# Kernel tuning notes

Hardware: AMD Instinct MI355X
Metric: run time of the kernel (lower is better)

The kernel has to match this reference:

```python
import jax, jax.numpy as jnp
import numpy as np

WINDOW = 8
HEADS = 8

def _rel_index(w):
    coords = np.stack(np.meshgrid(np.arange(w), np.arange(w), indexing='ij')).reshape(2, -1)
    rel = coords[:, :, None] - coords[:, None, :]          # [2, N, N]
    rel = rel.transpose(1, 2, 0) + (w - 1)                 # [N, N, 2]
    return jnp.asarray(rel[:, :, 0] * (2 * w - 1) + rel[:, :, 1])  # [N, N] int

def setup_inputs() -> dict:
    key = jax.random.key(0)
    ks = jax.random.split(key, 5)
    B, N, C = 4096, WINDOW * WINDOW, 256
    x = jax.random.normal(ks[0], (B, N, C), dtype=jnp.float32)
    w_qkv = jax.random.normal(ks[1], (3 * C, C), dtype=jnp.float32) * 0.02
    b_qkv = jnp.zeros((3 * C,), dtype=jnp.float32)
    bias_table = jax.random.normal(ks[2], ((2 * WINDOW - 1) ** 2, HEADS), dtype=jnp.float32) * 0.02
    w_proj = jax.random.normal(ks[3], (C, C), dtype=jnp.float32) * 0.02
    b_proj = jnp.zeros((C,), dtype=jnp.float32)
    return {"x": x, "w_qkv": w_qkv, "b_qkv": b_qkv, "bias_table": bias_table,
            "w_proj": w_proj, "b_proj": b_proj}

def reference(x, w_qkv, b_qkv, bias_table, w_proj, b_proj):
    B, N, C = x.shape
    H = HEADS
    d = C // H
    scale = d ** (-0.5)
    idx = _rel_index(WINDOW)                                # [N, N]
    qkv = x @ w_qkv.T + b_qkv                               # [B, N, 3C]
    qkv = qkv.reshape(B, N, 3, H, d).transpose(2, 0, 3, 1, 4)
    q, k, v = qkv[0], qkv[1], qkv[2]                        # [B, H, N, d]
    attn = jnp.einsum('bhnd,bhmd->bhnm', q * scale, k)      # [B, H, N, N]
    bias = bias_table[idx]                                  # [N, N, H]
    attn = attn + bias.transpose(2, 0, 1)[None]             # add per-head bias
    attn = jax.nn.softmax(attn, axis=-1)
    out = jnp.einsum('bhnm,bhmd->bhnd', attn, v)            # [B, H, N, d]
    out = out.transpose(0, 2, 1, 3).reshape(B, N, C)
    return out @ w_proj.T + b_proj
```

## Files before the change

### kernel.cpp

```cpp
#include <hip/hip_runtime.h>

typedef unsigned int u32;
typedef unsigned short u16;
typedef __bf16 bf16x8 __attribute__((ext_vector_type(8)));
typedef float f32x4 __attribute__((ext_vector_type(4)));
typedef u32 u32x4 __attribute__((ext_vector_type(4)));
typedef u32 u32x2 __attribute__((ext_vector_type(2)));

#define NTOK 64
#define CDIM 256
#define NH 8

#define WS_HDR 8
#define BIAS_O (WS_HDR)
#define WQKV_O (BIAS_O + 32768)
#define BQKV_O (WQKV_O + 196608)
#define WPRJ_O (BQKV_O + 768)
#define BPRJ_O (WPRJ_O + 65536)

#define XROW 520
#define XS_OFF 0
#define QS_OFF 33280
#define KS_OFF 66560
#define VT_OFF 99840
#define LDS_BYTES 134656

__device__ __forceinline__ float bf2f(u16 u) {
  union { u32 i; float f; } z; z.i = ((u32)u) << 16; return z.f;
}
__device__ __forceinline__ u16 f2bf(float f) {
  __bf16 h = (__bf16)f; return __builtin_bit_cast(u16, h);
}
__device__ __forceinline__ float fetchf(const void* p, int idx, int isbf) {
  return isbf ? bf2f(((const u16*)p)[idx]) : ((const float*)p)[idx];
}

__global__ void detect_dtype(const u16* __restrict__ x, int* __restrict__ flag) {
  __shared__ int cnt;
  if (threadIdx.x == 0) cnt = 0;
  __syncthreads();
  int sane = 0;
  for (int i = threadIdx.x; i < 2048; i += 256) {
    u16 u = x[2 * i];
    int e = (u >> 7) & 0xFF;
    sane += (e == 0 || (e >= 90 && e <= 160)) ? 1 : 0;
  }
  atomicAdd(&cnt, sane);
  __syncthreads();
  if (threadIdx.x == 0) *flag = (cnt >= 1638) ? 1 : 0;
}

__global__ void cvt_params(const void* __restrict__ wqkv, const void* __restrict__ bqkv,
                           const void* __restrict__ btab, const void* __restrict__ wprj,
                           const void* __restrict__ bprj, void* __restrict__ wsraw) {
  u16* ws = (u16*)wsraw;
  const int isbf = *(const int*)wsraw;
  int i = blockIdx.x * 256 + threadIdx.x;
  if (i < 32768) {
    int h = i >> 12, n = (i >> 6) & 63, m = i & 63;
    int r0 = (n >> 3) - (m >> 3) + 7, r1 = (n & 7) - (m & 7) + 7;
    ws[BIAS_O + (h << 12) + (m << 6) + n] = f2bf(fetchf(btab, (r0 * 15 + r1) * NH + h, isbf));
  } else if (i < 32768 + 196608) {
    int j = i - 32768;
    ws[WQKV_O + j] = f2bf(fetchf(wqkv, j, isbf));
  } else if (i < 32768 + 196608 + 768) {
    int j = i - (32768 + 196608);
    ws[BQKV_O + j] = f2bf(fetchf(bqkv, j, isbf));
  } else if (i < 32768 + 196608 + 768 + 65536) {
    int j = i - (32768 + 196608 + 768);
    ws[WPRJ_O + j] = f2bf(fetchf(wprj, j, isbf));
  } else if (i < 32768 + 196608 + 768 + 65536 + 256) {
    int j = i - (32768 + 196608 + 768 + 65536);
    ws[BPRJ_O + j] = f2bf(fetchf(bprj, j, isbf));
  }
}

__global__ __launch_bounds__(512, 2)
void win_attn_fused(const void* __restrict__ xraw, const void* __restrict__ wsraw,
                    float* __restrict__ out)
{
  __shared__ __align__(16) unsigned char lds[LDS_BYTES];
  const u16* ws  = (const u16*)wsraw;
  const int isbf = *(const int*)wsraw;
  const int b    = blockIdx.x;
  const int tid  = threadIdx.x;
  const int w    = tid >> 6;
  const int lane = tid & 63;
  const int c    = lane & 15;
  const int g    = lane >> 4;

  if (isbf) {
    const u32x4* gx = (const u32x4*)((const u16*)xraw + (size_t)b * (NTOK * CDIM));
#pragma unroll
    for (int i = 0; i < 4; ++i) {
      int q = tid + i * 512;
      int row = q >> 5, c8 = q & 31;
      *(u32x4*)(lds + XS_OFF + row * XROW + c8 * 16) = gx[q];
    }
  } else {
    const f32x4* gx = (const f32x4*)((const float*)xraw + (size_t)b * (NTOK * CDIM));
#pragma unroll
    for (int i = 0; i < 8; ++i) {
      int q = tid + i * 512;
      int row = q >> 6, c4 = q & 63;
      f32x4 v = gx[q];
      u32x2 pk;
      pk[0] = (u32)f2bf(v[0]) | ((u32)f2bf(v[1]) << 16);
      pk[1] = (u32)f2bf(v[2]) | ((u32)f2bf(v[3]) << 16);
      *(u32x2*)(lds + XS_OFF + row * XROW + c4 * 8) = pk;
    }
  }
  __syncthreads();

  const float scale = 0.1767766952966369f;

  {
    bf16x8 af[4][8];
#pragma unroll
    for (int rt = 0; rt < 4; ++rt)
#pragma unroll
      for (int ks = 0; ks < 8; ++ks)
        af[rt][ks] = *(const bf16x8*)(lds + XS_OFF + (16 * rt + c) * XROW + ks * 64 + g * 16);

    for (int jt = 0; jt < 6; ++jt) {
      const int jc   = w * 96 + jt * 16;
      const int colw = jc + c;
      f32x4 acc[4] = {{0,0,0,0},{0,0,0,0},{0,0,0,0},{0,0,0,0}};
      const u16* wrow = ws + WQKV_O + colw * CDIM;
#pragma unroll
      for (int ks = 0; ks < 8; ++ks) {
        bf16x8 bf = *(const bf16x8*)(wrow + ks * 32 + g * 8);
#pragma unroll
        for (int rt = 0; rt < 4; ++rt)
          acc[rt] = __builtin_amdgcn_mfma_f32_16x16x32_bf16(af[rt][ks], bf, acc[rt], 0, 0, 0);
      }
      const float badd = bf2f(ws[BQKV_O + colw]);
#pragma unroll
      for (int rt = 0; rt < 4; ++rt) {
#pragma unroll
        for (int reg = 0; reg < 4; ++reg) {
          int r = 16 * rt + 4 * g + reg;
          float val = acc[rt][reg] + badd;
          if (jc < 256) {
            *(u16*)(lds + QS_OFF + r * XROW + colw * 2) = f2bf(val * scale);
          } else if (jc < 512) {
            *(u16*)(lds + KS_OFF + r * XROW + (colw - 256) * 2) = f2bf(val);
          } else {
            int cc = colw - 512, hd = cc >> 5, dd = cc & 31;
            *(u16*)(lds + VT_OFF + hd * 4352 + dd * 136 + r * 2) = f2bf(val);
          }
        }
      }
    }
  }
  __syncthreads();

  const int h = w;
  f32x4 s[4][4];
#pragma unroll
  for (int rt = 0; rt < 4; ++rt)
#pragma unroll
    for (int ct = 0; ct < 4; ++ct) {
      u32x2 bp = *(const u32x2*)(ws + BIAS_O + (h << 12) + ((16 * ct + c) << 6) + 16 * rt + 4 * g);
      s[rt][ct][0] = bf2f((u16)(bp[0] & 0xffff));
      s[rt][ct][1] = bf2f((u16)(bp[0] >> 16));
      s[rt][ct][2] = bf2f((u16)(bp[1] & 0xffff));
      s[rt][ct][3] = bf2f((u16)(bp[1] >> 16));
    }
  {
    bf16x8 aq[4], bk[4];
#pragma unroll
    for (int rt = 0; rt < 4; ++rt)
      aq[rt] = *(const bf16x8*)(lds + QS_OFF + (16 * rt + c) * XROW + h * 64 + g * 16);
#pragma unroll
    for (int ct = 0; ct < 4; ++ct)
      bk[ct] = *(const bf16x8*)(lds + KS_OFF + (16 * ct + c) * XROW + h * 64 + g * 16);
#pragma unroll
    for (int rt = 0; rt < 4; ++rt)
#pragma unroll
      for (int ct = 0; ct < 4; ++ct)
        s[rt][ct] = __builtin_amdgcn_mfma_f32_16x16x32_bf16(aq[rt], bk[ct], s[rt][ct], 0, 0, 0);
  }

#pragma unroll
  for (int rt = 0; rt < 4; ++rt) {
#pragma unroll
    for (int reg = 0; reg < 4; ++reg) {
      float v0 = s[rt][0][reg], v1 = s[rt][1][reg], v2 = s[rt][2][reg], v3 = s[rt][3][reg];
      float mx = fmaxf(fmaxf(v0, v1), fmaxf(v2, v3));
#pragma unroll
      for (int i = 1; i < 16; i <<= 1) mx = fmaxf(mx, __shfl_xor(mx, i));
      v0 = __expf(v0 - mx); v1 = __expf(v1 - mx);
      v2 = __expf(v2 - mx); v3 = __expf(v3 - mx);
      float sm = v0 + v1 + v2 + v3;
#pragma unroll
      for (int i = 1; i < 16; i <<= 1) sm += __shfl_xor(sm, i);
      float inv = 1.0f / sm;
      s[rt][0][reg] = v0 * inv; s[rt][1][reg] = v1 * inv;
      s[rt][2][reg] = v2 * inv; s[rt][3][reg] = v3 * inv;
    }
  }
  __syncthreads();

  const int Pb = w * 8192;
#pragma unroll
  for (int rt = 0; rt < 4; ++rt)
#pragma unroll
    for (int ct = 0; ct < 4; ++ct)
#pragma unroll
      for (int reg = 0; reg < 4; ++reg) {
        int r = 16 * rt + 4 * g + reg, cc = 16 * ct + c;
        int byte = (r * 128 + cc * 2) ^ ((r & 7) << 4);
        *(u16*)(lds + Pb + byte) = f2bf(s[rt][ct][reg]);
      }
  asm volatile("" ::: "memory");

  f32x4 o[4][2] = {{{0,0,0,0},{0,0,0,0}},{{0,0,0,0},{0,0,0,0}},
                   {{0,0,0,0},{0,0,0,0}},{{0,0,0,0},{0,0,0,0}}};
#pragma unroll
  for (int ks = 0; ks < 2; ++ks) {
    bf16x8 ap[4], bv[2];
#pragma unroll
    for (int rt = 0; rt < 4; ++rt) {
      int r = 16 * rt + c;
      int byte = (r * 128 + ks * 64 + g * 16) ^ ((r & 7) << 4);
      ap[rt] = *(const bf16x8*)(lds + Pb + byte);
    }
#pragma unroll
    for (int ct = 0; ct < 2; ++ct)
      bv[ct] = *(const bf16x8*)(lds + VT_OFF + h * 4352 + (16 * ct + c) * 136 + ks * 64 + g * 16);
#pragma unroll
    for (int rt = 0; rt < 4; ++rt)
#pragma unroll
      for (int ct = 0; ct < 2; ++ct)
        o[rt][ct] = __builtin_amdgcn_mfma_f32_16x16x32_bf16(ap[rt], bv[ct], o[rt][ct], 0, 0, 0);
  }
#pragma unroll
  for (int rt = 0; rt < 4; ++rt)
#pragma unroll
    for (int ct = 0; ct < 2; ++ct)
#pragma unroll
      for (int reg = 0; reg < 4; ++reg) {
        int n = 16 * rt + 4 * g + reg;
        int col = h * 32 + 16 * ct + c;
        *(u16*)(lds + KS_OFF + n * XROW + col * 2) = f2bf(o[rt][ct][reg]);
      }
  __syncthreads();

  {
    bf16x8 ay[4][8];
#pragma unroll
    for (int rt = 0; rt < 4; ++rt)
#pragma unroll
      for (int ks = 0; ks < 8; ++ks)
        ay[rt][ks] = *(const bf16x8*)(lds + KS_OFF + (16 * rt + c) * XROW + ks * 64 + g * 16);

#pragma unroll
    for (int ct = 0; ct < 2; ++ct) {
      const int colw = w * 32 + ct * 16 + c;
      const float badd = bf2f(ws[BPRJ_O + colw]);
      f32x4 acc[4];
#pragma unroll
      for (int rt = 0; rt < 4; ++rt)
#pragma unroll
        for (int reg = 0; reg < 4; ++reg) acc[rt][reg] = badd;
      const u16* wrow = ws + WPRJ_O + colw * CDIM;
#pragma unroll
      for (int ks = 0; ks < 8; ++ks) {
        bf16x8 bf = *(const bf16x8*)(wrow + ks * 32 + g * 8);
#pragma unroll
        for (int rt = 0; rt < 4; ++rt)
          acc[rt] = __builtin_amdgcn_mfma_f32_16x16x32_bf16(ay[rt][ks], bf, acc[rt], 0, 0, 0);
      }
#pragma unroll
      for (int rt = 0; rt < 4; ++rt)
#pragma unroll
        for (int reg = 0; reg < 4; ++reg) {
          int n = 16 * rt + 4 * g + reg;
          int byte = (n * 1024 + colw * 4) ^ (((n >> 2) & 3) << 6);
          *(float*)(lds + byte) = acc[rt][reg];
        }
    }
  }
  __syncthreads();

  float* gout = out + (size_t)b * (NTOK * CDIM);
#pragma unroll
  for (int i = 0; i < 8; ++i) {
    int q = tid + i * 512;
    int row = q >> 6, c16 = q & 63;
    f32x4 v = *(const f32x4*)(lds + ((row * 1024 + c16 * 16) ^ (((row >> 2) & 3) << 6)));
    *(f32x4*)(gout + row * CDIM + c16 * 4) = v;
  }
}

extern "C" void kernel_launch(void* const* d_in, const int* in_sizes, int n_in,
                              void* d_out, int out_size, void* d_ws, size_t ws_size,
                              hipStream_t stream) {
  (void)in_sizes; (void)n_in; (void)out_size; (void)ws_size;
  detect_dtype<<<dim3(1), dim3(256), 0, stream>>>((const u16*)d_in[0], (int*)d_ws);
  cvt_params<<<dim3(1156), dim3(256), 0, stream>>>(d_in[1], d_in[2], d_in[3], d_in[4],
                                                   d_in[5], d_ws);
  win_attn_fused<<<dim3(4096), dim3(512), 0, stream>>>(d_in[0], d_ws, (float*)d_out);
}
```

Before: 556.1 us.

## Shrink LDS footprint: load x directly to registers, keep V in registers, direct stores

The kernel stops staging x and the transposed V in LDS. X fragments are loaded straight from global memory into MFMA registers, and V is kept packed in registers and redistributed with lane shuffles. The output projection is written directly to global memory instead of going through an LDS staging buffer. LDS use drops from about 134KB to 66KB, and launch bounds rise to 4 blocks per CU, so more waves can be resident. The cost is uncoalesced scalar fp32 global stores, extra shuffles, more register pressure, and the bias layout is reworked so S is computed transposed.

```diff
diff --git a/kernel.cpp b/kernel.cpp
--- a/kernel.cpp
+++ b/kernel.cpp
@@ -19,11 +19,9 @@
 #define BPRJ_O (WPRJ_O + 65536)
 
 #define XROW 520
-#define XS_OFF 0
-#define QS_OFF 33280
-#define KS_OFF 66560
-#define VT_OFF 99840
-#define LDS_BYTES 134656
+#define QS_OFF 0
+#define KS_OFF 33280
+#define LDS_BYTES 66560
 
 __device__ __forceinline__ float bf2f(u16 u) {
   union { u32 i; float f; } z; z.i = ((u32)u) << 16; return z.f;
@@ -57,9 +55,9 @@
   const int isbf = *(const int*)wsraw;
   int i = blockIdx.x * 256 + threadIdx.x;
   if (i < 32768) {
-    int h = i >> 12, n = (i >> 6) & 63, m = i & 63;
+    int n = (i >> 6) & 63, m = i & 63, h = i >> 12;
     int r0 = (n >> 3) - (m >> 3) + 7, r1 = (n & 7) - (m & 7) + 7;
-    ws[BIAS_O + (h << 12) + (m << 6) + n] = f2bf(fetchf(btab, (r0 * 15 + r1) * NH + h, isbf));
+    ws[BIAS_O + i] = f2bf(fetchf(btab, (r0 * 15 + r1) * NH + h, isbf));
   } else if (i < 32768 + 196608) {
     int j = i - 32768;
     ws[WQKV_O + j] = f2bf(fetchf(wqkv, j, isbf));
@@ -75,7 +73,7 @@
   }
 }
 
-__global__ __launch_bounds__(512, 2)
+__global__ __launch_bounds__(512, 4)
 void win_attn_fused(const void* __restrict__ xraw, const void* __restrict__ wsraw,
                     float* __restrict__ out)
 {
@@ -88,173 +86,195 @@
   const int lane = tid & 63;
   const int c    = lane & 15;
   const int g    = lane >> 4;
-
-  if (isbf) {
-    const u32x4* gx = (const u32x4*)((const u16*)xraw + (size_t)b * (NTOK * CDIM));
-#pragma unroll
-    for (int i = 0; i < 4; ++i) {
-      int q = tid + i * 512;
-      int row = q >> 5, c8 = q & 31;
-      *(u32x4*)(lds + XS_OFF + row * XROW + c8 * 16) = gx[q];
-    }
-  } else {
-    const f32x4* gx = (const f32x4*)((const float*)xraw + (size_t)b * (NTOK * CDIM));
-#pragma unroll
-    for (int i = 0; i < 8; ++i) {
-      int q = tid + i * 512;
-      int row = q >> 6, c4 = q & 63;
-      f32x4 v = gx[q];
-      u32x2 pk;
-      pk[0] = (u32)f2bf(v[0]) | ((u32)f2bf(v[1]) << 16);
-      pk[1] = (u32)f2bf(v[2]) | ((u32)f2bf(v[3]) << 16);
-      *(u32x2*)(lds + XS_OFF + row * XROW + c4 * 8) = pk;
-    }
-  }
-  __syncthreads();
-
   const float scale = 0.1767766952966369f;
 
+  u32 vpk[2][4][2];
+
   {
-    bf16x8 af[4][8];
-#pragma unroll
-    for (int rt = 0; rt < 4; ++rt)
-#pragma unroll
-      for (int ks = 0; ks < 8; ++ks)
-        af[rt][ks] = *(const bf16x8*)(lds + XS_OFF + (16 * rt + c) * XROW + ks * 64 + g * 16);
-
-    for (int jt = 0; jt < 6; ++jt) {
-      const int jc   = w * 96 + jt * 16;
-      const int colw = jc + c;
-      f32x4 acc[4] = {{0,0,0,0},{0,0,0,0},{0,0,0,0},{0,0,0,0}};
-      const u16* wrow = ws + WQKV_O + colw * CDIM;
-#pragma unroll
-      for (int ks = 0; ks < 8; ++ks) {
-        bf16x8 bf = *(const bf16x8*)(wrow + ks * 32 + g * 8);
-#pragma unroll
-        for (int rt = 0; rt < 4; ++rt)
-          acc[rt] = __builtin_amdgcn_mfma_f32_16x16x32_bf16(af[rt][ks], bf, acc[rt], 0, 0, 0);
-      }
-      const float badd = bf2f(ws[BQKV_O + colw]);
-#pragma unroll
-      for (int rt = 0; rt < 4; ++rt) {
-#pragma unroll
-        for (int reg = 0; reg < 4; ++reg) {
-          int r = 16 * rt + 4 * g + reg;
-          float val = acc[rt][reg] + badd;
-          if (jc < 256) {
-            *(u16*)(lds + QS_OFF + r * XROW + colw * 2) = f2bf(val * scale);
-          } else if (jc < 512) {
-            *(u16*)(lds + KS_OFF + r * XROW + (colw - 256) * 2) = f2bf(val);
+    const u16*   x16 = (const u16*)xraw + (size_t)b * (NTOK * CDIM);
+    const float* xf  = (const float*)xraw + (size_t)b * (NTOK * CDIM);
+#pragma unroll
+    for (int half = 0; half < 2; ++half) {
+      bf16x8 af[2][8];
+#pragma unroll
+      for (int rt2 = 0; rt2 < 2; ++rt2)
+#pragma unroll
+        for (int ks = 0; ks < 8; ++ks) {
+          const int off = (32 * half + 16 * rt2 + c) * CDIM + ks * 32 + g * 8;
+          if (isbf) {
+            af[rt2][ks] = *(const bf16x8*)(x16 + off);
           } else {
-            int cc = colw - 512, hd = cc >> 5, dd = cc & 31;
-            *(u16*)(lds + VT_OFF + hd * 4352 + dd * 136 + r * 2) = f2bf(val);
+            f32x4 lo = *(const f32x4*)(xf + off);
+            f32x4 hi = *(const f32x4*)(xf + off + 4);
+            u32x4 pk;
+            pk[0] = (u32)f2bf(lo[0]) | ((u32)f2bf(lo[1]) << 16);
+            pk[1] = (u32)f2bf(lo[2]) | ((u32)f2bf(lo[3]) << 16);
+            pk[2] = (u32)f2bf(hi[0]) | ((u32)f2bf(hi[1]) << 16);
+            pk[3] = (u32)f2bf(hi[2]) | ((u32)f2bf(hi[3]) << 16);
+            af[rt2][ks] = __builtin_bit_cast(bf16x8, pk);
           }
         }
+#pragma unroll
+      for (int t = 0; t < 3; ++t)
+#pragma unroll
+        for (int jt = 0; jt < 2; ++jt) {
+          const int lcol = w * 32 + jt * 16 + c;
+          const int colw = t * 256 + lcol;
+          f32x4 acc[2] = {{0,0,0,0},{0,0,0,0}};
+          const u16* wrow = ws + WQKV_O + colw * CDIM;
+#pragma unroll
+          for (int ks = 0; ks < 8; ++ks) {
+            bf16x8 bf = *(const bf16x8*)(wrow + ks * 32 + g * 8);
+            acc[0] = __builtin_amdgcn_mfma_f32_16x16x32_bf16(af[0][ks], bf, acc[0], 0, 0, 0);
+            acc[1] = __builtin_amdgcn_mfma_f32_16x16x32_bf16(af[1][ks], bf, acc[1], 0, 0, 0);
+          }
+          const float badd = bf2f(ws[BQKV_O + colw]);
+#pragma unroll
+          for (int rt2 = 0; rt2 < 2; ++rt2) {
+            if (t == 0) {
+#pragma unroll
+              for (int reg = 0; reg < 4; ++reg) {
+                int r = 32 * half + 16 * rt2 + 4 * g + reg;
+                *(u16*)(lds + QS_OFF + r * XROW + lcol * 2) = f2bf((acc[rt2][reg] + badd) * scale);
+              }
+            } else if (t == 1) {
+#pragma unroll
+              for (int reg = 0; reg < 4; ++reg) {
+                int r = 32 * half + 16 * rt2 + 4 * g + reg;
+                *(u16*)(lds + KS_OFF + r * XROW + lcol * 2) = f2bf(acc[rt2][reg] + badd);
+              }
+            } else {
+              vpk[jt][2 * half + rt2][0] =
+                  (u32)f2bf(acc[rt2][0] + badd) | ((u32)f2bf(acc[rt2][1] + badd) << 16);
+              vpk[jt][2 * half + rt2][1] =
+                  (u32)f2bf(acc[rt2][2] + badd) | ((u32)f2bf(acc[rt2][3] + badd) << 16);
+            }
+          }
+        }
+    }
+  }
+  asm volatile("" ::: "memory");
+
+  bf16x8 bk[4], aq[4];
+#pragma unroll
+  for (int rt = 0; rt < 4; ++rt)
+    bk[rt] = *(const bf16x8*)(lds + KS_OFF + (16 * rt + c) * XROW + w * 64 + g * 16);
+#pragma unroll
+  for (int ct = 0; ct < 4; ++ct)
+    aq[ct] = *(const bf16x8*)(lds + QS_OFF + (16 * ct + c) * XROW + w * 64 + g * 16);
+  __syncthreads();
+
+  f32x4 sT[4][4];
+#pragma unroll
+  for (int rt = 0; rt < 4; ++rt)
+#pragma unroll
+    for (int ct = 0; ct < 4; ++ct) {
+      u32x2 bp = *(const u32x2*)(ws + BIAS_O + (w << 12) + ((16 * ct + c) << 6) + 16 * rt + 4 * g);
+      sT[rt][ct][0] = bf2f((u16)(bp[0] & 0xffff));
+      sT[rt][ct][1] = bf2f((u16)(bp[0] >> 16));
+      sT[rt][ct][2] = bf2f((u16)(bp[1] & 0xffff));
+      sT[rt][ct][3] = bf2f((u16)(bp[1] >> 16));
+    }
+#pragma unroll
+  for (int rt = 0; rt < 4; ++rt)
+#pragma unroll
+    for (int ct = 0; ct < 4; ++ct)
+      sT[rt][ct] = __builtin_amdgcn_mfma_f32_16x16x32_bf16(bk[rt], aq[ct], sT[rt][ct], 0, 0, 0);
+
+#pragma unroll
+  for (int ct = 0; ct < 4; ++ct) {
+    float mx = sT[0][ct][0];
+#pragma unroll
+    for (int rt = 0; rt < 4; ++rt)
+#pragma unroll
+      for (int reg = 0; reg < 4; ++reg) mx = fmaxf(mx, sT[rt][ct][reg]);
+    mx = fmaxf(mx, __shfl_xor(mx, 16));
+    mx = fmaxf(mx, __shfl_xor(mx, 32));
+    float sum = 0.f;
+#pragma unroll
+    for (int rt = 0; rt < 4; ++rt)
+#pragma unroll
+      for (int reg = 0; reg < 4; ++reg) {
+        float e = __expf(sT[rt][ct][reg] - mx);
+        sT[rt][ct][reg] = e; sum += e;
       }
-    }
-  }
-  __syncthreads();
-
-  const int h = w;
-  f32x4 s[4][4];
+    sum += __shfl_xor(sum, 16);
+    sum += __shfl_xor(sum, 32);
+    float inv = 1.0f / sum;
+#pragma unroll
+    for (int rt = 0; rt < 4; ++rt)
+#pragma unroll
+      for (int reg = 0; reg < 4; ++reg) sT[rt][ct][reg] *= inv;
+  }
+
+  const int Pb = w * 8192;
 #pragma unroll
   for (int rt = 0; rt < 4; ++rt)
 #pragma unroll
     for (int ct = 0; ct < 4; ++ct) {
-      u32x2 bp = *(const u32x2*)(ws + BIAS_O + (h << 12) + ((16 * ct + c) << 6) + 16 * rt + 4 * g);
-      s[rt][ct][0] = bf2f((u16)(bp[0] & 0xffff));
-      s[rt][ct][1] = bf2f((u16)(bp[0] >> 16));
-      s[rt][ct][2] = bf2f((u16)(bp[1] & 0xffff));
-      s[rt][ct][3] = bf2f((u16)(bp[1] >> 16));
-    }
-  {
-    bf16x8 aq[4], bk[4];
-#pragma unroll
-    for (int rt = 0; rt < 4; ++rt)
-      aq[rt] = *(const bf16x8*)(lds + QS_OFF + (16 * rt + c) * XROW + h * 64 + g * 16);
-#pragma unroll
-    for (int ct = 0; ct < 4; ++ct)
-      bk[ct] = *(const bf16x8*)(lds + KS_OFF + (16 * ct + c) * XROW + h * 64 + g * 16);
-#pragma unroll
-    for (int rt = 0; rt < 4; ++rt)
-#pragma unroll
-      for (int ct = 0; ct < 4; ++ct)
-        s[rt][ct] = __builtin_amdgcn_mfma_f32_16x16x32_bf16(aq[rt], bk[ct], s[rt][ct], 0, 0, 0);
-  }
-
-#pragma unroll
-  for (int rt = 0; rt < 4; ++rt) {
-#pragma unroll
-    for (int reg = 0; reg < 4; ++reg) {
-      float v0 = s[rt][0][reg], v1 = s[rt][1][reg], v2 = s[rt][2][reg], v3 = s[rt][3][reg];
-      float mx = fmaxf(fmaxf(v0, v1), fmaxf(v2, v3));
-#pragma unroll
-      for (int i = 1; i < 16; i <<= 1) mx = fmaxf(mx, __shfl_xor(mx, i));
-      v0 = __expf(v0 - mx); v1 = __expf(v1 - mx);
-      v2 = __expf(v2 - mx); v3 = __expf(v3 - mx);
-      float sm = v0 + v1 + v2 + v3;
-#pragma unroll
-      for (int i = 1; i < 16; i <<= 1) sm += __shfl_xor(sm, i);
-      float inv = 1.0f / sm;
-      s[rt][0][reg] = v0 * inv; s[rt][1][reg] = v1 * inv;
-      s[rt][2][reg] = v2 * inv; s[rt][3][reg] = v3 * inv;
-    }
-  }
-  __syncthreads();
-
-  const int Pb = w * 8192;
-#pragma unroll
-  for (int rt = 0; rt < 4; ++rt)
-#pragma unroll
-    for (int ct = 0; ct < 4; ++ct)
-#pragma unroll
-      for (int reg = 0; reg < 4; ++reg) {
-        int r = 16 * rt + 4 * g + reg, cc = 16 * ct + c;
-        int byte = (r * 128 + cc * 2) ^ ((r & 7) << 4);
-        *(u16*)(lds + Pb + byte) = f2bf(s[rt][ct][reg]);
-      }
+      int n = 16 * ct + c;
+      int byte = (n * 128 + 32 * rt + 8 * g) ^ ((n & 7) << 4);
+      u32x2 pk;
+      pk[0] = (u32)f2bf(sT[rt][ct][0]) | ((u32)f2bf(sT[rt][ct][1]) << 16);
+      pk[1] = (u32)f2bf(sT[rt][ct][2]) | ((u32)f2bf(sT[rt][ct][3]) << 16);
+      *(u32x2*)(lds + Pb + byte) = pk;
+    }
   asm volatile("" ::: "memory");
+
+  bf16x8 bv[2][2];
+#pragma unroll
+  for (int ct2 = 0; ct2 < 2; ++ct2)
+#pragma unroll
+    for (int ks = 0; ks < 2; ++ks) {
+      const int s0 = c + 32 * (g & 1), s1 = s0 + 16;
+      u32 A0 = (u32)__shfl((int)vpk[ct2][2 * ks    ][0], s0, 64);
+      u32 A1 = (u32)__shfl((int)vpk[ct2][2 * ks    ][1], s0, 64);
+      u32 B0 = (u32)__shfl((int)vpk[ct2][2 * ks + 1][0], s0, 64);
+      u32 B1 = (u32)__shfl((int)vpk[ct2][2 * ks + 1][1], s0, 64);
+      u32 C0 = (u32)__shfl((int)vpk[ct2][2 * ks    ][0], s1, 64);
+      u32 C1 = (u32)__shfl((int)vpk[ct2][2 * ks    ][1], s1, 64);
+      u32 D0 = (u32)__shfl((int)vpk[ct2][2 * ks + 1][0], s1, 64);
+      u32 D1 = (u32)__shfl((int)vpk[ct2][2 * ks + 1][1], s1, 64);
+      const bool hi = (g >> 1) & 1;
+      u32x4 f;
+      f[0] = hi ? B0 : A0;  f[1] = hi ? B1 : A1;
+      f[2] = hi ? D0 : C0;  f[3] = hi ? D1 : C1;
+      bv[ct2][ks] = __builtin_bit_cast(bf16x8, f);
+    }
 
   f32x4 o[4][2] = {{{0,0,0,0},{0,0,0,0}},{{0,0,0,0},{0,0,0,0}},
                    {{0,0,0,0},{0,0,0,0}},{{0,0,0,0},{0,0,0,0}}};
 #pragma unroll
-  for (int ks = 0; ks < 2; ++ks) {
-    bf16x8 ap[4], bv[2];
+  for (int ks = 0; ks < 2; ++ks)
 #pragma unroll
     for (int rt = 0; rt < 4; ++rt) {
-      int r = 16 * rt + c;
-      int byte = (r * 128 + ks * 64 + g * 16) ^ ((r & 7) << 4);
-      ap[rt] = *(const bf16x8*)(lds + Pb + byte);
-    }
-#pragma unroll
-    for (int ct = 0; ct < 2; ++ct)
-      bv[ct] = *(const bf16x8*)(lds + VT_OFF + h * 4352 + (16 * ct + c) * 136 + ks * 64 + g * 16);
-#pragma unroll
-    for (int rt = 0; rt < 4; ++rt)
-#pragma unroll
-      for (int ct = 0; ct < 2; ++ct)
-        o[rt][ct] = __builtin_amdgcn_mfma_f32_16x16x32_bf16(ap[rt], bv[ct], o[rt][ct], 0, 0, 0);
-  }
-#pragma unroll
-  for (int rt = 0; rt < 4; ++rt)
-#pragma unroll
-    for (int ct = 0; ct < 2; ++ct)
+      int n = 16 * rt + c;
+      bf16x8 pa = *(const bf16x8*)(lds + Pb + ((n * 128 + 64 * ks + 16 * g) ^ ((n & 7) << 4)));
+      o[rt][0] = __builtin_amdgcn_mfma_f32_16x16x32_bf16(pa, bv[0][ks], o[rt][0], 0, 0, 0);
+      o[rt][1] = __builtin_amdgcn_mfma_f32_16x16x32_bf16(pa, bv[1][ks], o[rt][1], 0, 0, 0);
+    }
+  __syncthreads();
+
+#pragma unroll
+  for (int rt = 0; rt < 4; ++rt)
+#pragma unroll
+    for (int ct2 = 0; ct2 < 2; ++ct2)
 #pragma unroll
       for (int reg = 0; reg < 4; ++reg) {
         int n = 16 * rt + 4 * g + reg;
-        int col = h * 32 + 16 * ct + c;
-        *(u16*)(lds + KS_OFF + n * XROW + col * 2) = f2bf(o[rt][ct][reg]);
+        int col = w * 32 + 16 * ct2 + c;
+        *(u16*)(lds + n * XROW + col * 2) = f2bf(o[rt][ct2][reg]);
       }
   __syncthreads();
 
+  float* gout = out + (size_t)b * (NTOK * CDIM);
   {
     bf16x8 ay[4][8];
 #pragma unroll
     for (int rt = 0; rt < 4; ++rt)
 #pragma unroll
       for (int ks = 0; ks < 8; ++ks)
-        ay[rt][ks] = *(const bf16x8*)(lds + KS_OFF + (16 * rt + c) * XROW + ks * 64 + g * 16);
-
+        ay[rt][ks] = *(const bf16x8*)(lds + (16 * rt + c) * XROW + ks * 64 + g * 16);
 #pragma unroll
     for (int ct = 0; ct < 2; ++ct) {
       const int colw = w * 32 + ct * 16 + c;
@@ -277,20 +297,9 @@
 #pragma unroll
         for (int reg = 0; reg < 4; ++reg) {
           int n = 16 * rt + 4 * g + reg;
-          int byte = (n * 1024 + colw * 4) ^ (((n >> 2) & 3) << 6);
-          *(float*)(lds + byte) = acc[rt][reg];
+          gout[n * CDIM + colw] = acc[rt][reg];
         }
     }
-  }
-  __syncthreads();
-
-  float* gout = out + (size_t)b * (NTOK * CDIM);
-#pragma unroll
-  for (int i = 0; i < 8; ++i) {
-    int q = tid + i * 512;
-    int row = q >> 6, c16 = q & 63;
-    f32x4 v = *(const f32x4*)(lds + ((row * 1024 + c16 * 16) ^ (((row >> 2) & 3) << 6)));
-    *(f32x4*)(gout + row * CDIM + c16 * 4) = v;
   }
 }
 
```

After: 1.361 ms. 2.45x slower.
